# Performance work log

Hardware: AMD Instinct MI355X
Metric: run time of the kernel (lower is better)

Reference implementation:

```python
import jax, jax.numpy as jnp
import numpy as np

HEADS = 8
DH = 64          # channel_head
HID = HEADS * DH # 512
QC = 256         # query_channel


def rmsnorm(x, g):
    # lucidrains-style RMSNorm over channel dim of [b, c, h, w]:
    # F.normalize(x, dim=1) * g * sqrt(C)
    n = jnp.sqrt(jnp.sum(x * x, axis=1, keepdims=True))
    x = x / jnp.maximum(n, 1e-12)
    return x * (x.shape[1] ** 0.5) * g[None, :, None, None]


def setup_inputs() -> dict:
    key = jax.random.key(0)
    ks = jax.random.split(key, 6)
    B, H, W = 8, 64, 64
    x = jax.random.normal(ks[0], (B, QC, H, W), dtype=jnp.float32)
    Wq = jax.random.normal(ks[1], (HID, QC), dtype=jnp.float32) * 0.02
    Wk = jax.random.normal(ks[2], (HID, QC), dtype=jnp.float32) * 0.02
    Wv = jax.random.normal(ks[3], (HID, QC), dtype=jnp.float32) * 0.02
    conv_w = jax.random.normal(ks[4], (QC, HID), dtype=jnp.float32) * 0.02  # 1x1 conv
    conv_b = jnp.zeros((QC,), dtype=jnp.float32)
    g_ffn = jnp.ones((QC,), dtype=jnp.float32)
    g_norm = jnp.ones((QC,), dtype=jnp.float32)
    return {"x": x, "Wq": Wq, "Wk": Wk, "Wv": Wv, "conv_w": conv_w,
            "conv_b": conv_b, "g_ffn": g_ffn, "g_norm": g_norm}


def reference(x, Wq, Wk, Wv, conv_w, conv_b, g_ffn, g_norm):
    b, c, h, w = x.shape
    n = h * w
    xn = rmsnorm(x, g_norm)                    # pre-norm; residual uses xn (x_in)
    t = xn.reshape(b, c, n).transpose(0, 2, 1)  # [b, n, c]
    q = t @ Wq.T                                # [b, n, HID]
    k = t @ Wk.T
    v = t @ Wv.T
    split = lambda z: z.reshape(b, n, HEADS, DH).transpose(0, 2, 1, 3)  # [b,h,n,d]
    q, k, v = split(q), split(k), split(v)
    q = jax.nn.softmax(q, axis=-1) * (DH ** -0.5)  # softmax over d, then scale
    k = jax.nn.softmax(k, axis=-2)                 # softmax over n
    attn = jnp.einsum('bhnd,bhne->bhde', k, v)     # K^T V, [b,h,d,d]
    out = jnp.einsum('bhnd,bhde->bhne', q, attn)   # [b,h,n,d]
    out = out.transpose(0, 2, 1, 3).reshape(b, n, HID)
    out = out.transpose(0, 2, 1).reshape(b, HID, h, w)
    out = jnp.einsum('bchw,oc->bohw', out, conv_w) + conv_b[None, :, None, None]
    out = rmsnorm(out, g_ffn)
    return out + xn
```

## Files before the change

### kernel.cpp

```cpp
#include <hip/hip_runtime.h>
#include <hip/hip_bf16.h>

#define B_ 8
#define C_ 256
#define N_ 4096
#define HID_ 512

typedef __bf16 bf16;
typedef bf16 bf16x8 __attribute__((ext_vector_type(8)));
typedef bf16 bf16x4 __attribute__((ext_vector_type(4)));
typedef float f32x4 __attribute__((ext_vector_type(4)));

#define T_OFF    0u
#define U_OFF    16777216u
#define S_OFF    17825792u
#define M2T_OFF  17973248u
#define WQ_OFF   20070400u
#define WK_OFF   20332544u
#define WV_OFF   20594688u

__device__ __forceinline__ f32x4 mfma16(bf16x8 a, bf16x8 b, f32x4 c) {
    return __builtin_amdgcn_mfma_f32_16x16x32_bf16(a, b, c, 0, 0, 0);
}

__device__ __forceinline__ void gload_lds16(const void* g, void* l) {
    __builtin_amdgcn_global_load_lds(
        (const __attribute__((address_space(1))) unsigned int*)g,
        (__attribute__((address_space(3))) unsigned int*)l, 16, 0, 0);
}

__global__ void __launch_bounds__(256, 4) k_nc(const float* __restrict__ x,
                                               const float* __restrict__ gnorm,
                                               bf16* __restrict__ t,
                                               const float* __restrict__ wq,
                                               const float* __restrict__ wk,
                                               const float* __restrict__ wv,
                                               bf16* __restrict__ oq,
                                               bf16* __restrict__ ok,
                                               bf16* __restrict__ ov,
                                               float* __restrict__ uz) {
    __shared__ float part[4][64];
    __shared__ __align__(16) bf16 tbuf[64 * 256];
    if (blockIdx.x >= 704) {
        const f32x4 z = {0.f, 0.f, 0.f, 0.f};
        int idx = (blockIdx.x - 704) * 256 + threadIdx.x;
        f32x4* dst = (f32x4*)uz;
#pragma unroll
        for (int i = 0; i < 9; ++i) {
            int j = idx + i * 8192;
            if (j < 66560) dst[j] = z;
        }
        return;
    }
    if (blockIdx.x >= 512) {
        int bb = blockIdx.x - 512;
        int m = bb >> 6;
        const float* src = (m == 0) ? wq : ((m == 1) ? wk : wv);
        bf16* dst = (m == 0) ? oq : ((m == 1) ? ok : ov);
        int tid = threadIdx.x;
        int i0 = ((bb & 63) * 256 + tid) * 8;
        f32x4 a = *(const f32x4*)(src + i0);
        f32x4 b2 = *(const f32x4*)(src + i0 + 4);
        bf16x8 o;
#pragma unroll
        for (int j = 0; j < 4; ++j) { o[j] = (bf16)a[j]; o[j + 4] = (bf16)b2[j]; }
        int row = (bb & 63) * 8 + (tid >> 5);
        int k0 = (tid & 31) * 8;
        int p = row >> 4, l15 = row & 15;
        int ks = k0 >> 5, g = (k0 >> 3) & 3;
        *(bf16x8*)(dst + ((size_t)((p * 8 + ks) * 64 + g * 16 + l15)) * 8) = o;
        return;
    }
    int b = blockIdx.x >> 6;
    int chunk = blockIdx.x & 63;
    int p = threadIdx.x & 63;
    int cq = threadIdx.x >> 6;
    int pix = (chunk << 6) + p;
    const float* xb = x + (size_t)b * C_ * N_ + (size_t)(cq * 64) * N_ + pix;
    float xv[64];
    float ss = 0.f;
#pragma unroll
    for (int c = 0; c < 64; ++c) { xv[c] = xb[(size_t)c * N_]; ss += xv[c] * xv[c]; }
    part[cq][p] = ss;
    __syncthreads();
    float tot = part[0][p] + part[1][p] + part[2][p] + part[3][p];
    float s = 16.0f / fmaxf(sqrtf(tot), 1e-12f);
#pragma unroll
    for (int c0 = 0; c0 < 64; c0 += 8) {
        bf16x8 pk;
#pragma unroll
        for (int j = 0; j < 8; ++j)
            pk[j] = (bf16)(xv[c0 + j] * s * gnorm[cq * 64 + c0 + j]);
        int cbyte = cq * 128 + c0 * 2;
        *(bf16x8*)((char*)tbuf + p * 512 + (cbyte ^ ((p & 7) << 4))) = pk;
    }
    __syncthreads();
    char* gt = (char*)(t + ((size_t)(b * N_ + (chunk << 6))) * 256);
#pragma unroll
    for (int it = 0; it < 8; ++it) {
        int o = it * 4096 + threadIdx.x * 16;
        int src = o ^ (((o >> 9) & 7) << 4);
        *(f32x4*)(gt + o) = *(const f32x4*)((const char*)tbuf + src);
    }
}

__global__ void __launch_bounds__(256, 2) k_kv(const bf16* __restrict__ t,
                                               const bf16* __restrict__ wkb,
                                               const bf16* __restrict__ wvb,
                                               float* __restrict__ U,
                                               float* __restrict__ S) {
    __shared__ __align__(16) bf16 tS[64 * 256];
    __shared__ __align__(16) bf16 ekT[64][72];
    __shared__ __align__(16) bf16 vT[64][72];
    int h = blockIdx.x >> 6;
    int b = (blockIdx.x >> 3) & 7;
    int chunk = blockIdx.x & 7;
    int w = threadIdx.x >> 6;
    int l = threadIdx.x & 63;
    int l15 = l & 15, g = l >> 4;
    int xorm = (l15 & 7) << 4;

    const bf16* wsel = (w < 2) ? wkb : wvb;
    int c0 = (w & 1) * 32;
    bool isk = (w < 2);
    bf16x8 wf[2][8];
#pragma unroll
    for (int nf = 0; nf < 2; ++nf) {
        int pp = h * 4 + (w & 1) * 2 + nf;
#pragma unroll
        for (int ks = 0; ks < 8; ++ks)
            wf[nf][ks] = *(const bf16x8*)(wsel + ((size_t)((pp * 8 + ks) * 64 + l)) * 8);
    }

    const f32x4 fz = {0.f, 0.f, 0.f, 0.f};
    f32x4 uacc[4];
#pragma unroll
    for (int df = 0; df < 4; ++df) uacc[df] = fz;
    float sreg = 0.f;

    size_t rowbase = (size_t)b * N_ + chunk * 512;
    for (int tile = 0; tile < 8; ++tile) {
        {
            const char* gt = (const char*)(t + (rowbase + tile * 64) * 256);
#pragma unroll
            for (int it = 0; it < 8; ++it) {
                int o = it * 4096 + w * 1024 + l * 16;
                int src = o ^ (((o >> 9) & 7) << 4);
                gload_lds16(gt + src, (char*)tS + it * 4096 + w * 1024);
            }
        }
        __syncthreads();
        f32x4 acc[4][2];
#pragma unroll
        for (int mf = 0; mf < 4; ++mf) { acc[mf][0] = fz; acc[mf][1] = fz; }
#pragma unroll
        for (int ks = 0; ks < 8; ++ks) {
#pragma unroll
            for (int mf = 0; mf < 4; ++mf) {
                bf16x8 a = *(const bf16x8*)((const char*)tS + (mf * 16 + l15) * 512 + ((ks * 64 + g * 16) ^ xorm));
                acc[mf][0] = mfma16(a, wf[0][ks], acc[mf][0]);
                acc[mf][1] = mfma16(a, wf[1][ks], acc[mf][1]);
            }
        }
        __syncthreads();
#pragma unroll
        for (int mf = 0; mf < 4; ++mf)
#pragma unroll
            for (int nf = 0; nf < 2; ++nf) {
                int cc = c0 + nf * 16 + l15;
                int rr = mf * 16 + g * 4;
                bf16x4 pk;
#pragma unroll
                for (int r = 0; r < 4; ++r) {
                    float v = acc[mf][nf][r];
                    pk[r] = (bf16)(isk ? __expf(v) : v);
                }
                if (isk) *(bf16x4*)(&ekT[cc][rr]) = pk;
                else     *(bf16x4*)(&vT[cc][rr]) = pk;
            }
        __syncthreads();
#pragma unroll
        for (int k2 = 0; k2 < 2; ++k2) {
            bf16x8 bv = *(const bf16x8*)(&vT[w * 16 + l15][k2 * 32 + g * 8]);
#pragma unroll
            for (int df = 0; df < 4; ++df) {
                bf16x8 ae = *(const bf16x8*)(&ekT[df * 16 + l15][k2 * 32 + g * 8]);
                uacc[df] = mfma16(ae, bv, uacc[df]);
            }
        }
        {
#pragma unroll
            for (int i = 0; i < 16; ++i) sreg += (float)ekT[l][w * 16 + i];
        }
    }
    int bh = b * 8 + h;
    float* Ubh = U + (size_t)bh * 4096;
#pragma unroll
    for (int df = 0; df < 4; ++df)
#pragma unroll
        for (int r = 0; r < 4; ++r)
            atomicAdd(Ubh + (df * 16 + g * 4 + r) * 64 + w * 16 + l15, uacc[df][r]);
    atomicAdd(S + bh * 64 + l, sreg);
}

__global__ void __launch_bounds__(256) k_attn_m2(const float* __restrict__ U,
                                                 const float* __restrict__ S,
                                                 const float* __restrict__ cw,
                                                 bf16* __restrict__ m2t) {
    __shared__ float at[16][64];
    int b = blockIdx.x & 7, dq = (blockIdx.x >> 3) & 3, h = blockIdx.x >> 5;
    int tid = threadIdx.x;
    const float* Ub = U + (size_t)(b * 8 + h) * 4096 + dq * 16 * 64;
    const float* Sb = S + (b * 8 + h) * 64 + dq * 16;
    for (int it = 0; it < 4; ++it) {
        int idx = it * 256 + tid;
        at[idx >> 6][idx & 63] = Ub[idx] / Sb[idx >> 6];
    }
    __syncthreads();
    int o = tid;
    float cwr[64];
#pragma unroll
    for (int e = 0; e < 64; ++e) cwr[e] = cw[(size_t)o * 512 + h * 64 + e];
    bf16* mb = m2t + (size_t)b * 131072;
    int pp = o >> 4, l15o = o & 15;
#pragma unroll
    for (int j0 = 0; j0 < 16; j0 += 8) {
        bf16x8 pk;
#pragma unroll
        for (int j = 0; j < 8; ++j) {
            float a2 = 0.f;
#pragma unroll
            for (int e = 0; e < 64; ++e) a2 += at[j0 + j][e] * cwr[e];
            pk[j] = (bf16)a2;
        }
        int kk = dq * 16 + j0;
        int ksg = h * 2 + (kk >> 5);
        int gg = (kk >> 3) & 3;
        *(bf16x8*)(mb + ((size_t)((pp * 16 + ksg) * 64 + gg * 16 + l15o)) * 8) = pk;
    }
}

__global__ void __launch_bounds__(512, 4) k_qout(const bf16* __restrict__ t,
                                                 const bf16* __restrict__ wqb,
                                                 const bf16* __restrict__ m2t,
                                                 const float* __restrict__ gffn,
                                                 const float* __restrict__ cb,
                                                 float* __restrict__ out) {
    __shared__ __align__(16) char smem[66560 + 2048];
    bf16 (*qsm)[520] = (bf16(*)[520])smem;
    float* rowsum = (float*)(smem + 66560);
    bf16* tS = (bf16*)smem;
    int b = blockIdx.x & 7;
    int row0 = (blockIdx.x >> 3) << 6;
    int tid = threadIdx.x;
    int w = tid >> 6, l = tid & 63;
    int l15 = l & 15, g = l >> 4;
    int xorm = (l15 & 7) << 4;
    const f32x4 fz = {0.f, 0.f, 0.f, 0.f};

    {
        const char* gt = (const char*)(t + (size_t)(b * N_ + row0) * 256);
#pragma unroll
        for (int it = 0; it < 4; ++it) {
            int o = it * 8192 + tid * 16;
            int src = o ^ (((o >> 9) & 7) << 4);
            gload_lds16(gt + src, (char*)tS + o);
        }
    }
    __syncthreads();

    f32x4 acc[4][4];
#pragma unroll
    for (int mf = 0; mf < 4; ++mf)
#pragma unroll
        for (int nf = 0; nf < 4; ++nf) acc[mf][nf] = fz;
#pragma unroll
    for (int ks = 0; ks < 8; ++ks) {
        bf16x8 a[4];
#pragma unroll
        for (int mf = 0; mf < 4; ++mf)
            a[mf] = *(const bf16x8*)((const char*)tS + (mf * 16 + l15) * 512 + ((ks * 64 + g * 16) ^ xorm));
#pragma unroll
        for (int nf = 0; nf < 4; ++nf) {
            bf16x8 bq = *(const bf16x8*)(wqb + ((size_t)(((w * 4 + nf) * 8 + ks) * 64 + l)) * 8);
#pragma unroll
            for (int mf = 0; mf < 4; ++mf)
                acc[mf][nf] = mfma16(a[mf], bq, acc[mf][nf]);
        }
    }
    __syncthreads();

#pragma unroll
    for (int mf = 0; mf < 4; ++mf)
#pragma unroll
        for (int r = 0; r < 4; ++r) {
            float mx = -1e30f;
#pragma unroll
            for (int nf = 0; nf < 4; ++nf) mx = fmaxf(mx, acc[mf][nf][r]);
            mx = fmaxf(mx, __shfl_xor(mx, 1));
            mx = fmaxf(mx, __shfl_xor(mx, 2));
            mx = fmaxf(mx, __shfl_xor(mx, 4));
            mx = fmaxf(mx, __shfl_xor(mx, 8));
            float p[4]; float sm = 0.f;
#pragma unroll
            for (int nf = 0; nf < 4; ++nf) { p[nf] = __expf(acc[mf][nf][r] - mx); sm += p[nf]; }
            sm += __shfl_xor(sm, 1);
            sm += __shfl_xor(sm, 2);
            sm += __shfl_xor(sm, 4);
            sm += __shfl_xor(sm, 8);
            float scl = 0.125f / sm;
            int row = mf * 16 + g * 4 + r;
#pragma unroll
            for (int nf = 0; nf < 4; ++nf)
                qsm[row][w * 64 + nf * 16 + l15] = (bf16)(p[nf] * scl);
        }
    __syncthreads();

    f32x4 acc2[4][2];
#pragma unroll
    for (int mf = 0; mf < 4; ++mf)
#pragma unroll
        for (int nf = 0; nf < 2; ++nf) acc2[mf][nf] = fz;
    const bf16* mb = m2t + (size_t)b * 131072;
#pragma unroll
    for (int ks = 0; ks < 16; ++ks) {
        bf16x8 a[4];
#pragma unroll
        for (int mf = 0; mf < 4; ++mf)
            a[mf] = *(const bf16x8*)(&qsm[mf * 16 + l15][ks * 32 + g * 8]);
#pragma unroll
        for (int nf = 0; nf < 2; ++nf) {
            bf16x8 bm = *(const bf16x8*)(mb + ((size_t)(((w * 2 + nf) * 16 + ks) * 64 + l)) * 8);
#pragma unroll
            for (int mf = 0; mf < 4; ++mf)
                acc2[mf][nf] = mfma16(a[mf], bm, acc2[mf][nf]);
        }
    }

#pragma unroll
    for (int nf = 0; nf < 2; ++nf) {
        float bias = cb[w * 32 + nf * 16 + l15];
#pragma unroll
        for (int mf = 0; mf < 4; ++mf)
#pragma unroll
            for (int r = 0; r < 4; ++r) acc2[mf][nf][r] += bias;
    }
#pragma unroll
    for (int mf = 0; mf < 4; ++mf)
#pragma unroll
        for (int r = 0; r < 4; ++r) {
            float ssq = 0.f;
#pragma unroll
            for (int nf = 0; nf < 2; ++nf) ssq += acc2[mf][nf][r] * acc2[mf][nf][r];
            ssq += __shfl_xor(ssq, 1);
            ssq += __shfl_xor(ssq, 2);
            ssq += __shfl_xor(ssq, 4);
            ssq += __shfl_xor(ssq, 8);
            if (l15 == 0) rowsum[w * 64 + mf * 16 + g * 4 + r] = ssq;
        }
    __syncthreads();
    float sclr[4][4];
#pragma unroll
    for (int mf = 0; mf < 4; ++mf)
#pragma unroll
        for (int r = 0; r < 4; ++r) {
            int row = mf * 16 + g * 4 + r;
            float tot = 0.f;
#pragma unroll
            for (int ww = 0; ww < 8; ++ww) tot += rowsum[ww * 64 + row];
            sclr[mf][r] = 16.0f / fmaxf(sqrtf(tot), 1e-12f);
        }

    float* obuf = (float*)smem;
    const bf16* gtb = t + (size_t)(b * N_ + row0) * 256;
#pragma unroll
    for (int nf = 0; nf < 2; ++nf) {
        int col = w * 32 + nf * 16 + l15;
        float gf = gffn[col];
#pragma unroll
        for (int mf = 0; mf < 4; ++mf)
#pragma unroll
            for (int r = 0; r < 4; ++r) {
                int row = mf * 16 + g * 4 + r;
                float res = (float)gtb[row * 256 + col];
                obuf[col * 65 + row] = acc2[mf][nf][r] * sclr[mf][r] * gf + res;
            }
    }
    __syncthreads();
#pragma unroll
    for (int cc = 0; cc < 8; ++cc) {
        int c = cc * 32 + (tid >> 4);
        int j = (tid & 15) * 4;
        f32x4 v;
#pragma unroll
        for (int r = 0; r < 4; ++r) v[r] = obuf[c * 65 + j + r];
        __builtin_nontemporal_store(v, (f32x4*)(out + ((size_t)(b * 256 + c)) * N_ + row0 + j));
    }
}

extern "C" void kernel_launch(void* const* d_in, const int* in_sizes, int n_in,
                              void* d_out, int out_size, void* d_ws, size_t ws_size,
                              hipStream_t stream) {
    const float* x     = (const float*)d_in[0];
    const float* Wq    = (const float*)d_in[1];
    const float* Wk    = (const float*)d_in[2];
    const float* Wv    = (const float*)d_in[3];
    const float* cw    = (const float*)d_in[4];
    const float* cb    = (const float*)d_in[5];
    const float* gffn  = (const float*)d_in[6];
    const float* gnorm = (const float*)d_in[7];
    char* ws = (char*)d_ws;
    bf16* t    = (bf16*)(ws + T_OFF);
    float* U   = (float*)(ws + U_OFF);
    float* S   = (float*)(ws + S_OFF);
    bf16* m2t  = (bf16*)(ws + M2T_OFF);
    bf16* wqb  = (bf16*)(ws + WQ_OFF);
    bf16* wkb  = (bf16*)(ws + WK_OFF);
    bf16* wvb  = (bf16*)(ws + WV_OFF);
    float* out = (float*)d_out;

    k_nc<<<736, 256, 0, stream>>>(x, gnorm, t, Wq, Wk, Wv, wqb, wkb, wvb, U);
    k_kv<<<512, 256, 0, stream>>>(t, wkb, wvb, U, S);
    k_attn_m2<<<256, 256, 0, stream>>>(U, S, cw, m2t);
    k_qout<<<512, 512, 0, stream>>>(t, wqb, m2t, gffn, cb, out);
}
```

Baseline: 89.18 us.

## Process two heads per k_kv block to reuse each loaded t tile

Each k_kv block now computes two heads over a 256-row chunk instead of one head over a 512-row chunk, so the grid size stays the same. Each t tile staged into LDS is reused for both heads' K/V projections and K^T V accumulation. This halves how many times the t activations are re-read from global memory. In exchange, the per-thread weight fragments and U accumulators double, which raises register pressure and risks lower occupancy or spills.

Result: slower. 96.95 us (+8.7%).

```diff
diff --git a/kernel.cpp b/kernel.cpp
--- a/kernel.cpp
+++ b/kernel.cpp
@@ -112,9 +112,9 @@
     __shared__ __align__(16) bf16 tS[64 * 256];
     __shared__ __align__(16) bf16 ekT[64][72];
     __shared__ __align__(16) bf16 vT[64][72];
-    int h = blockIdx.x >> 6;
-    int b = (blockIdx.x >> 3) & 7;
-    int chunk = blockIdx.x & 7;
+    int hp = blockIdx.x >> 7;
+    int b = (blockIdx.x >> 4) & 7;
+    int chunk = blockIdx.x & 15;
     int w = threadIdx.x >> 6;
     int l = threadIdx.x & 63;
     int l15 = l & 15, g = l >> 4;
@@ -123,23 +123,29 @@
     const bf16* wsel = (w < 2) ? wkb : wvb;
     int c0 = (w & 1) * 32;
     bool isk = (w < 2);
-    bf16x8 wf[2][8];
-#pragma unroll
-    for (int nf = 0; nf < 2; ++nf) {
-        int pp = h * 4 + (w & 1) * 2 + nf;
-#pragma unroll
-        for (int ks = 0; ks < 8; ++ks)
-            wf[nf][ks] = *(const bf16x8*)(wsel + ((size_t)((pp * 8 + ks) * 64 + l)) * 8);
+    bf16x8 wf[2][2][8];
+#pragma unroll
+    for (int hh = 0; hh < 2; ++hh) {
+        int h = hp * 2 + hh;
+#pragma unroll
+        for (int nf = 0; nf < 2; ++nf) {
+            int pp = h * 4 + (w & 1) * 2 + nf;
+#pragma unroll
+            for (int ks = 0; ks < 8; ++ks)
+                wf[hh][nf][ks] = *(const bf16x8*)(wsel + ((size_t)((pp * 8 + ks) * 64 + l)) * 8);
+        }
     }
 
     const f32x4 fz = {0.f, 0.f, 0.f, 0.f};
-    f32x4 uacc[4];
-#pragma unroll
-    for (int df = 0; df < 4; ++df) uacc[df] = fz;
-    float sreg = 0.f;
-
-    size_t rowbase = (size_t)b * N_ + chunk * 512;
-    for (int tile = 0; tile < 8; ++tile) {
+    f32x4 uacc[2][4];
+#pragma unroll
+    for (int hh = 0; hh < 2; ++hh)
+#pragma unroll
+        for (int df = 0; df < 4; ++df) uacc[hh][df] = fz;
+    float sreg[2] = {0.f, 0.f};
+
+    size_t rowbase = (size_t)b * N_ + chunk * 256;
+    for (int tile = 0; tile < 4; ++tile) {
         {
             const char* gt = (const char*)(t + (rowbase + tile * 64) * 256);
 #pragma unroll
@@ -150,57 +156,65 @@
             }
         }
         __syncthreads();
-        f32x4 acc[4][2];
-#pragma unroll
-        for (int mf = 0; mf < 4; ++mf) { acc[mf][0] = fz; acc[mf][1] = fz; }
-#pragma unroll
-        for (int ks = 0; ks < 8; ++ks) {
-#pragma unroll
-            for (int mf = 0; mf < 4; ++mf) {
-                bf16x8 a = *(const bf16x8*)((const char*)tS + (mf * 16 + l15) * 512 + ((ks * 64 + g * 16) ^ xorm));
-                acc[mf][0] = mfma16(a, wf[0][ks], acc[mf][0]);
-                acc[mf][1] = mfma16(a, wf[1][ks], acc[mf][1]);
+#pragma unroll
+        for (int hh = 0; hh < 2; ++hh) {
+            f32x4 acc[4][2];
+#pragma unroll
+            for (int mf = 0; mf < 4; ++mf) { acc[mf][0] = fz; acc[mf][1] = fz; }
+#pragma unroll
+            for (int ks = 0; ks < 8; ++ks) {
+#pragma unroll
+                for (int mf = 0; mf < 4; ++mf) {
+                    bf16x8 a = *(const bf16x8*)((const char*)tS + (mf * 16 + l15) * 512 + ((ks * 64 + g * 16) ^ xorm));
+                    acc[mf][0] = mfma16(a, wf[hh][0][ks], acc[mf][0]);
+                    acc[mf][1] = mfma16(a, wf[hh][1][ks], acc[mf][1]);
+                }
             }
-        }
-        __syncthreads();
-#pragma unroll
-        for (int mf = 0; mf < 4; ++mf)
-#pragma unroll
-            for (int nf = 0; nf < 2; ++nf) {
-                int cc = c0 + nf * 16 + l15;
-                int rr = mf * 16 + g * 4;
-                bf16x4 pk;
-#pragma unroll
-                for (int r = 0; r < 4; ++r) {
-                    float v = acc[mf][nf][r];
-                    pk[r] = (bf16)(isk ? __expf(v) : v);
+            __syncthreads();
+#pragma unroll
+            for (int mf = 0; mf < 4; ++mf)
+#pragma unroll
+                for (int nf = 0; nf < 2; ++nf) {
+                    int cc = c0 + nf * 16 + l15;
+                    int rr = mf * 16 + g * 4;
+                    bf16x4 pk;
+#pragma unroll
+                    for (int r = 0; r < 4; ++r) {
+                        float v = acc[mf][nf][r];
+                        pk[r] = (bf16)(isk ? __expf(v) : v);
+                    }
+                    if (isk) *(bf16x4*)(&ekT[cc][rr]) = pk;
+                    else     *(bf16x4*)(&vT[cc][rr]) = pk;
                 }
-                if (isk) *(bf16x4*)(&ekT[cc][rr]) = pk;
-                else     *(bf16x4*)(&vT[cc][rr]) = pk;
+            __syncthreads();
+#pragma unroll
+            for (int k2 = 0; k2 < 2; ++k2) {
+                bf16x8 bv = *(const bf16x8*)(&vT[w * 16 + l15][k2 * 32 + g * 8]);
+#pragma unroll
+                for (int df = 0; df < 4; ++df) {
+                    bf16x8 ae = *(const bf16x8*)(&ekT[df * 16 + l15][k2 * 32 + g * 8]);
+                    uacc[hh][df] = mfma16(ae, bv, uacc[hh][df]);
+                }
             }
-        __syncthreads();
-#pragma unroll
-        for (int k2 = 0; k2 < 2; ++k2) {
-            bf16x8 bv = *(const bf16x8*)(&vT[w * 16 + l15][k2 * 32 + g * 8]);
-#pragma unroll
-            for (int df = 0; df < 4; ++df) {
-                bf16x8 ae = *(const bf16x8*)(&ekT[df * 16 + l15][k2 * 32 + g * 8]);
-                uacc[df] = mfma16(ae, bv, uacc[df]);
+            {
+                float s8 = 0.f;
+#pragma unroll
+                for (int i = 0; i < 16; ++i) s8 += (float)ekT[l][w * 16 + i];
+                sreg[hh] += s8;
             }
         }
-        {
-#pragma unroll
-            for (int i = 0; i < 16; ++i) sreg += (float)ekT[l][w * 16 + i];
-        }
-    }
-    int bh = b * 8 + h;
-    float* Ubh = U + (size_t)bh * 4096;
-#pragma unroll
-    for (int df = 0; df < 4; ++df)
-#pragma unroll
-        for (int r = 0; r < 4; ++r)
-            atomicAdd(Ubh + (df * 16 + g * 4 + r) * 64 + w * 16 + l15, uacc[df][r]);
-    atomicAdd(S + bh * 64 + l, sreg);
+    }
+#pragma unroll
+    for (int hh = 0; hh < 2; ++hh) {
+        int bh = b * 8 + hp * 2 + hh;
+        float* Ubh = U + (size_t)bh * 4096;
+#pragma unroll
+        for (int df = 0; df < 4; ++df)
+#pragma unroll
+            for (int r = 0; r < 4; ++r)
+                atomicAdd(Ubh + (df * 16 + g * 4 + r) * 64 + w * 16 + l15, uacc[hh][df][r]);
+        atomicAdd(S + bh * 64 + l, sreg[hh]);
+    }
 }
 
 __global__ void __launch_bounds__(256) k_attn_m2(const float* __restrict__ U,
```
